# Performance work log

Measured on AMD Instinct MI355X. Metric: run time of the kernel, lower is better.

The kernel has to match this reference:

```python
import jax, jax.numpy as jnp
import numpy as np

K = 4096
CIN = 256


def _kaiming_uniform(key, shape):
    # torch kaiming_uniform_ default: gain=sqrt(2), bound = gain*sqrt(3/fan_in)
    fan_in = shape[1]
    bound = np.sqrt(6.0 / fan_in)
    return jax.random.uniform(key, shape, jnp.float32, -bound, bound)


def _linear_weight(key, shape):
    # torch nn.Linear default init: U(-1/sqrt(fan_in), 1/sqrt(fan_in))
    bound = 1.0 / np.sqrt(shape[1])
    return jax.random.uniform(key, shape, jnp.float32, -bound, bound)


def setup_inputs() -> dict:
    key = jax.random.key(0)
    k0, k1, k2, k3, k4 = jax.random.split(key, 5)
    latent = jax.random.normal(k0, (16, CIN, 32, 32), jnp.float32)
    temperature = jnp.float32(1.0)
    codebook = _kaiming_uniform(k1, (K, CIN))
    wq = _linear_weight(k2, (CIN, CIN))
    wk = _linear_weight(k3, (CIN, CIN))
    wv = _linear_weight(k4, (CIN, CIN))
    return {"latent": latent, "temperature": temperature, "codebook": codebook,
            "wq": wq, "wk": wk, "wv": wv}


def reference(latent, temperature, codebook, wq, wk, wv):
    # deterministic=True, additionWeight=True, dropout=None
    cin = latent.shape[1]
    scale = jnp.sqrt(jnp.asarray(cin, latent.dtype))
    q = jnp.einsum('nchw,dc->nhwd', latent, wq)      # [n,h,w,cin], Linear: x @ W^T
    kmat = codebook @ wk.T                           # [k,cin]
    v = codebook @ wv.T                              # [k,cin]
    logit = jnp.einsum('nhwc,kc->nhwk', q, kmat) / scale
    soft = jax.nn.softmax(logit, axis=-1)
    idx = jnp.argmax(logit, axis=-1)                 # [n,h,w]
    soft_v = jnp.einsum('nhwk,kc->nhwc', soft, v)
    hard_v = v[idx]                                  # one-hot @ v == gather
    result = jax.lax.stop_gradient(hard_v - soft_v) + soft_v
    quantized = jnp.transpose(result, (0, 3, 1, 2))  # [n,cin,h,w]
    return (quantized, idx.astype(jnp.uint8), logit, v)
```

## Files before the change

### kernel.cpp

```cpp
#include <hip/hip_runtime.h>
#include <math.h>
#include <float.h>

#define CIN 256
#define KCB 4096
#define NPOS 16384

#define OFF_QUANT 0
#define OFF_IDX   4194304
#define OFF_LOGIT 4210688
#define OFF_V     71319552

#define MARGIN 5e-4f

typedef short bf16x8 __attribute__((ext_vector_type(8)));
typedef float f32x4 __attribute__((ext_vector_type(4)));

__device__ __forceinline__ unsigned short rne_bf16(float x) {
  const unsigned u = __float_as_uint(x);
  return (unsigned short)((u + 0x7FFFu + ((u >> 16) & 1u)) >> 16);
}

__device__ __forceinline__ void gload_lds16(const void* g, void* l) {
  __builtin_amdgcn_global_load_lds(
      (const __attribute__((address_space(1))) unsigned int*)g,
      (__attribute__((address_space(3))) unsigned int*)l, 16, 0, 0);
}

__device__ __forceinline__ void top2_merge(float& m1, int& i1, float& m2,
                                           float om1, int oi1, float om2) {
  if (om1 > m1 || (om1 == m1 && oi1 < i1)) {
    m2 = fmaxf(m1, om2);
    m1 = om1;
    i1 = oi1;
  } else {
    m2 = fmaxf(m2, fmaxf(om1, om2));
  }
}

__global__ __launch_bounds__(256) void kvq_kernel(
    const float* __restrict__ cb, const float* __restrict__ wk,
    const float* __restrict__ wv, const float* __restrict__ latent,
    const float* __restrict__ wq, unsigned short* __restrict__ kb,
    float* __restrict__ kf, float* __restrict__ vout,
    unsigned short* __restrict__ qb, float* __restrict__ qf) {
  __shared__ float sh[16][CIN];
  const int t = threadIdx.x;
  if (blockIdx.x < 256) {
    const int k0 = blockIdx.x * 16;
#pragma unroll
    for (int i = 0; i < 16; ++i)
      sh[i][t] = cb[(size_t)(k0 + i) * CIN + t];
    __syncthreads();
    float acck[16], accv[16];
#pragma unroll
    for (int r = 0; r < 16; ++r) { acck[r] = 0.f; accv[r] = 0.f; }
    const float* wkr = wk + (size_t)t * CIN;
    const float* wvr = wv + (size_t)t * CIN;
    for (int j4 = 0; j4 < CIN; j4 += 4) {
      const float4 a4 = *(const float4*)&wkr[j4];
      const float4 b4 = *(const float4*)&wvr[j4];
      const float ae[4] = {a4.x, a4.y, a4.z, a4.w};
      const float be[4] = {b4.x, b4.y, b4.z, b4.w};
#pragma unroll
      for (int e = 0; e < 4; ++e) {
        const int j = j4 + e;
#pragma unroll
        for (int r = 0; r < 16; ++r) {
          const float c = sh[r][j];
          acck[r] = fmaf(c, ae[e], acck[r]);
          accv[r] = fmaf(c, be[e], accv[r]);
        }
      }
    }
#pragma unroll
    for (int r = 0; r < 16; ++r) {
      const float xk = acck[r];
      kb[(size_t)(k0 + r) * CIN + t] = rne_bf16(xk);
      kf[(size_t)(k0 + r) * CIN + t] = xk;
      vout[(size_t)(k0 + r) * CIN + t] = accv[r];
    }
  } else {
    const int p0 = (blockIdx.x - 256) * 16;
    const int n = p0 >> 10, hw0 = p0 & 1023;
    const float* lbase =
        latent + (size_t)n * (CIN * 1024) + (size_t)t * 1024 + hw0;
#pragma unroll
    for (int i4 = 0; i4 < 4; ++i4) {
      float4 v4 = *(const float4*)(lbase + i4 * 4);
      sh[i4 * 4 + 0][t] = v4.x;
      sh[i4 * 4 + 1][t] = v4.y;
      sh[i4 * 4 + 2][t] = v4.z;
      sh[i4 * 4 + 3][t] = v4.w;
    }
    __syncthreads();
    float acc[16];
#pragma unroll
    for (int r = 0; r < 16; ++r) acc[r] = 0.f;
    const float* wqr = wq + (size_t)t * CIN;
    for (int j4 = 0; j4 < CIN; j4 += 4) {
      const float4 w4 = *(const float4*)&wqr[j4];
      const float we[4] = {w4.x, w4.y, w4.z, w4.w};
#pragma unroll
      for (int e = 0; e < 4; ++e) {
        const int j = j4 + e;
#pragma unroll
        for (int r = 0; r < 16; ++r) acc[r] = fmaf(sh[r][j], we[e], acc[r]);
      }
    }
#pragma unroll
    for (int r = 0; r < 16; ++r) {
      qb[(size_t)(p0 + r) * CIN + t] = rne_bf16(acc[r]);
      qf[(size_t)(p0 + r) * CIN + t] = acc[r];
    }
  }
}

__global__ __launch_bounds__(256, 4) void logit_kernel(
    const unsigned short* __restrict__ qb, const unsigned short* __restrict__ kb,
    float* __restrict__ logit, float* __restrict__ pm1,
    int* __restrict__ pi1, float* __restrict__ pm2) {
  __shared__ __align__(16) unsigned short smem[2][2][128 * 32];

  const int t = threadIdx.x;
  const int b = blockIdx.x;
  const int x = (b & 7) * 512 + (b >> 3);
  const int bn = x & 31, bm = x >> 5;
  const int n0 = bn * 128, m0 = bm * 128;

  const int lane = t & 63, w = t >> 6;
  const int wr = w >> 1, wc = w & 1;
  const int fr = lane & 15, fq = lane >> 4;

  const int srow = t >> 2;
  const int spc = t & 3;
  const int slog = spc ^ ((srow >> 1) & 3);
  const int sldse = srow * 32 + spc * 8;

  int aoff[4], boff[4];
#pragma unroll
  for (int mi = 0; mi < 4; ++mi) {
    const int ar = wr * 64 + mi * 16 + fr;
    aoff[mi] = ar * 32 + (fq ^ ((ar >> 1) & 3)) * 8;
  }
#pragma unroll
  for (int ni = 0; ni < 4; ++ni) {
    const int br = wc * 64 + ni * 16 + fr;
    boff[ni] = br * 32 + (fq ^ ((br >> 1) & 3)) * 8;
  }

  f32x4 acc[4][4];
#pragma unroll
  for (int i = 0; i < 4; ++i)
#pragma unroll
    for (int j = 0; j < 4; ++j) acc[i][j] = (f32x4)(0.f);

#pragma unroll
  for (int h = 0; h < 2; ++h) {
    const int r = h * 64 + srow;
    gload_lds16(qb + (size_t)(m0 + r) * CIN + slog * 8,
                &smem[0][0][h * 2048 + sldse]);
    gload_lds16(kb + (size_t)(n0 + r) * CIN + slog * 8,
                &smem[0][1][h * 2048 + sldse]);
  }
  asm volatile("s_waitcnt vmcnt(0)" ::: "memory");
  __syncthreads();

  for (int s = 0; s < 8; ++s) {
    const int buf = s & 1;
    if (s < 7) {
      const int k0 = (s + 1) * 32;
      const int nb = buf ^ 1;
#pragma unroll
      for (int h = 0; h < 2; ++h) {
        const int r = h * 64 + srow;
        gload_lds16(qb + (size_t)(m0 + r) * CIN + k0 + slog * 8,
                    &smem[nb][0][h * 2048 + sldse]);
        gload_lds16(kb + (size_t)(n0 + r) * CIN + k0 + slog * 8,
                    &smem[nb][1][h * 2048 + sldse]);
      }
    }
    bf16x8 a[4], bfr[4];
#pragma unroll
    for (int mi = 0; mi < 4; ++mi) a[mi] = *(const bf16x8*)&smem[buf][0][aoff[mi]];
#pragma unroll
    for (int ni = 0; ni < 4; ++ni) bfr[ni] = *(const bf16x8*)&smem[buf][1][boff[ni]];
#pragma unroll
    for (int mi = 0; mi < 4; ++mi)
#pragma unroll
      for (int ni = 0; ni < 4; ++ni)
        acc[mi][ni] = __builtin_amdgcn_mfma_f32_16x16x32_bf16(
            a[mi], bfr[ni], acc[mi][ni], 0, 0, 0);
    asm volatile("s_waitcnt vmcnt(0)" ::: "memory");
    __syncthreads();
  }

  const float sc = 0.0625f;
  float* S1 = (float*)&smem[0][0][0];
  unsigned* S2 = (unsigned*)((char*)&smem[0][0][0] + 16384);
#pragma unroll
  for (int mi = 0; mi < 4; ++mi)
#pragma unroll
    for (int i = 0; i < 4; ++i) {
      const int rt = wr * 64 + mi * 16 + fq * 4 + i;
      const int row = m0 + rt;
      float vals[4];
#pragma unroll
      for (int ni = 0; ni < 4; ++ni) {
        vals[ni] = acc[mi][ni][i] * sc;
        __builtin_nontemporal_store(
            vals[ni], &logit[(size_t)row * KCB + n0 + wc * 64 + ni * 16 + fr]);
      }
      float m1 = vals[0], m2 = -FLT_MAX;
      int ni1 = 0;
#pragma unroll
      for (int ni = 1; ni < 4; ++ni) {
        if (vals[ni] > m1) { m2 = m1; m1 = vals[ni]; ni1 = ni; }
        else if (vals[ni] > m2) m2 = vals[ni];
      }
      const int sb = (wc * 128 + rt) * 16 + fr;
      S1[sb] = m1;
      S2[sb] = (__float_as_uint(m2) & ~3u) | (unsigned)ni1;
    }
  __syncthreads();
  if (t < 128) {
    float m1 = -FLT_MAX, m2 = -FLT_MAX;
    int i1 = 0;
#pragma unroll
    for (int wc2 = 0; wc2 < 2; ++wc2)
#pragma unroll
      for (int f4 = 0; f4 < 4; ++f4) {
        const int base = (wc2 * 128 + t) * 16 + f4 * 4;
        const float4 am1 = *(const float4*)&S1[base];
        const uint4 au2 = *(const uint4*)&S2[base];
        const unsigned ue[4] = {au2.x, au2.y, au2.z, au2.w};
        const float me[4] = {am1.x, am1.y, am1.z, am1.w};
#pragma unroll
        for (int e = 0; e < 4; ++e) {
          const int col = wc2 * 64 + (int)(ue[e] & 3u) * 16 + f4 * 4 + e;
          top2_merge(m1, i1, m2, me[e], col, __uint_as_float(ue[e] & ~3u));
        }
      }
    pm1[(size_t)(m0 + t) * 32 + bn] = m1;
    pi1[(size_t)(m0 + t) * 32 + bn] = n0 + i1;
    pm2[(size_t)(m0 + t) * 32 + bn] = m2;
  }
}

__global__ __launch_bounds__(256) void finish_kernel(
    const float* __restrict__ pm1, const int* __restrict__ pi1,
    const float* __restrict__ pm2, const float* __restrict__ logit,
    const float* __restrict__ qf, const float* __restrict__ kf,
    const float* __restrict__ vout, float* __restrict__ outq,
    float* __restrict__ outidx) {
  __shared__ float s_rowmax[16];
  __shared__ int s_rowidx[16];
  __shared__ int s_flag[16];
  __shared__ int s_nflag;
  __shared__ int s_cnt[4];
  __shared__ int s_list[4][64];

  const int t = threadIdx.x;
  const int p0 = blockIdx.x * 16;
  if (t == 0) s_nflag = 0;
  __syncthreads();

  {
    const int r = t >> 4, l16 = t & 15;
    const int p = p0 + r;
    const size_t base = (size_t)p * 32;
    float m1 = pm1[base + l16], m2 = pm2[base + l16];
    int i1 = pi1[base + l16];
    top2_merge(m1, i1, m2, pm1[base + 16 + l16], pi1[base + 16 + l16],
               pm2[base + 16 + l16]);
#pragma unroll
    for (int mask = 1; mask < 16; mask <<= 1) {
      const float om1 = __shfl_xor(m1, mask, 64);
      const int oi1 = __shfl_xor(i1, mask, 64);
      const float om2 = __shfl_xor(m2, mask, 64);
      top2_merge(m1, i1, m2, om1, oi1, om2);
    }
    if (l16 == 0) {
      s_rowidx[r] = i1;
      s_rowmax[r] = m1;
      if (m1 - m2 <= MARGIN) {
        const int pos = atomicAdd(&s_nflag, 1);
        s_flag[pos] = r;
      }
    }
  }
  __syncthreads();

  const int w = t >> 6, lane = t & 63;
  const int nf = s_nflag;
  for (int fi = w; fi < nf; fi += 4) {
    const int rloc = s_flag[fi];
    const int p = p0 + rloc;
    const float4 qv = *(const float4*)&qf[(size_t)p * CIN + lane * 4];
    if (lane == 0) s_cnt[w] = 0;
    const float thr = s_rowmax[rloc] - MARGIN;
    const float* lrow = logit + (size_t)p * KCB;
    for (int it = 0; it < 16; ++it) {
      const float4 xv = *(const float4*)&lrow[lane * 4 + it * 256];
      const float xe[4] = {xv.x, xv.y, xv.z, xv.w};
#pragma unroll
      for (int e = 0; e < 4; ++e) {
        if (xe[e] > thr) {
          const int pos = atomicAdd(&s_cnt[w], 1);
          if (pos < 64) s_list[w][pos] = lane * 4 + it * 256 + e;
        }
      }
    }
    const int nc = min(s_cnt[w], 64);
    float bestv = -FLT_MAX;
    int bestj = 0x7fffffff;
    for (int ci = 0; ci < nc; ++ci) {
      const int j = s_list[w][ci];
      const float4 kv4 = *(const float4*)&kf[(size_t)j * CIN + lane * 4];
      float d = qv.x * kv4.x + qv.y * kv4.y + qv.z * kv4.z + qv.w * kv4.w;
#pragma unroll
      for (int m = 1; m < 64; m <<= 1) d += __shfl_xor(d, m, 64);
      const float val = d * 0.0625f;
      if (val > bestv || (val == bestv && j < bestj)) { bestv = val; bestj = j; }
    }
    if (lane == 0) s_rowidx[rloc] = bestj;
  }
  __syncthreads();

  const int n = p0 >> 10, hw0 = p0 & 1023;
  float res[16];
#pragma unroll
  for (int r2 = 0; r2 < 16; ++r2)
    res[r2] = vout[(size_t)s_rowidx[r2] * CIN + t];
  float* ob = outq + (size_t)n * (CIN * 1024) + (size_t)t * 1024 + hw0;
#pragma unroll
  for (int i4 = 0; i4 < 4; ++i4)
    *(float4*)&ob[i4 * 4] = make_float4(res[i4 * 4 + 0], res[i4 * 4 + 1],
                                        res[i4 * 4 + 2], res[i4 * 4 + 3]);
  if (t < 16) outidx[p0 + t] = (float)(s_rowidx[t] & 255);
}

extern "C" void kernel_launch(void* const* d_in, const int* in_sizes, int n_in,
                              void* d_out, int out_size, void* d_ws,
                              size_t ws_size, hipStream_t stream) {
  const float* latent = (const float*)d_in[0];
  const float* codebook = (const float*)d_in[2];
  const float* wq = (const float*)d_in[3];
  const float* wk = (const float*)d_in[4];
  const float* wv = (const float*)d_in[5];

  float* out = (float*)d_out;
  float* outq = out + OFF_QUANT;
  float* outidx = out + OFF_IDX;
  float* outlogit = out + OFF_LOGIT;
  float* outv = out + OFF_V;

  char* ws = (char*)d_ws;
  unsigned short* qb = (unsigned short*)(ws + 0);
  unsigned short* kb = (unsigned short*)(ws + 8388608);
  float* kf = (float*)(ws + 10485760);
  float* pm1 = (float*)(ws + 14680064);
  int* pi1 = (int*)(ws + 16777216);
  float* pm2 = (float*)(ws + 18874368);
  float* qf = (float*)(ws + 20971520);

  kvq_kernel<<<256 + NPOS / 16, 256, 0, stream>>>(codebook, wk, wv, latent, wq,
                                                  kb, kf, outv, qb, qf);
  logit_kernel<<<4096, 256, 0, stream>>>(qb, kb, outlogit, pm1, pi1, pm2);
  finish_kernel<<<NPOS / 16, 256, 0, stream>>>(pm1, pi1, pm2, outlogit, qf, kf,
                                               outv, outq, outidx);
}
```

Before: 167.0 us.

## Fuse finish stage into logit kernel via last-block-per-panel atomic counter

Removes the separate finish kernel launch. Each logit block increments a per-row-panel counter after writing its partial top-2 results. The last of the 32 column blocks for a panel then does the argmax reduction, the near-tie rescoring and the quantized/index writes for those 128 rows. This saves a launch and lets the finish work overlap the tail of the logit GEMM. In exchange, the finish work per panel is serialized in a single block and extra threadfences are added. The counters are zeroed in the first kernel.

```diff
diff --git a/kernel.cpp b/kernel.cpp
--- a/kernel.cpp
+++ b/kernel.cpp
@@ -43,9 +43,11 @@
     const float* __restrict__ wv, const float* __restrict__ latent,
     const float* __restrict__ wq, unsigned short* __restrict__ kb,
     float* __restrict__ kf, float* __restrict__ vout,
-    unsigned short* __restrict__ qb, float* __restrict__ qf) {
+    unsigned short* __restrict__ qb, float* __restrict__ qf,
+    int* __restrict__ panel_cnt) {
   __shared__ float sh[16][CIN];
   const int t = threadIdx.x;
+  if (blockIdx.x == 0 && t < 128) panel_cnt[t] = 0;
   if (blockIdx.x < 256) {
     const int k0 = blockIdx.x * 16;
 #pragma unroll
@@ -119,7 +121,10 @@
 __global__ __launch_bounds__(256, 4) void logit_kernel(
     const unsigned short* __restrict__ qb, const unsigned short* __restrict__ kb,
     float* __restrict__ logit, float* __restrict__ pm1,
-    int* __restrict__ pi1, float* __restrict__ pm2) {
+    int* __restrict__ pi1, float* __restrict__ pm2,
+    const float* __restrict__ qf, const float* __restrict__ kf,
+    const float* __restrict__ vout, float* __restrict__ outq,
+    float* __restrict__ outidx, int* __restrict__ panel_cnt) {
   __shared__ __align__(16) unsigned short smem[2][2][128 * 32];
 
   const int t = threadIdx.x;
@@ -245,14 +250,17 @@
     pi1[(size_t)(m0 + t) * 32 + bn] = n0 + i1;
     pm2[(size_t)(m0 + t) * 32 + bn] = m2;
   }
-}
-
-__global__ __launch_bounds__(256) void finish_kernel(
-    const float* __restrict__ pm1, const int* __restrict__ pi1,
-    const float* __restrict__ pm2, const float* __restrict__ logit,
-    const float* __restrict__ qf, const float* __restrict__ kf,
-    const float* __restrict__ vout, float* __restrict__ outq,
-    float* __restrict__ outidx) {
+  __syncthreads();
+
+  __shared__ int s_last;
+  if (t == 0) {
+    __threadfence();
+    s_last = (atomicAdd(&panel_cnt[bm], 1) == 31) ? 1 : 0;
+  }
+  __syncthreads();
+  if (!s_last) return;
+  __threadfence();
+
   __shared__ float s_rowmax[16];
   __shared__ int s_rowidx[16];
   __shared__ int s_flag[16];
@@ -260,84 +268,92 @@
   __shared__ int s_cnt[4];
   __shared__ int s_list[4][64];
 
-  const int t = threadIdx.x;
-  const int p0 = blockIdx.x * 16;
-  if (t == 0) s_nflag = 0;
-  __syncthreads();
-
-  {
-    const int r = t >> 4, l16 = t & 15;
-    const int p = p0 + r;
-    const size_t base = (size_t)p * 32;
-    float m1 = pm1[base + l16], m2 = pm2[base + l16];
-    int i1 = pi1[base + l16];
-    top2_merge(m1, i1, m2, pm1[base + 16 + l16], pi1[base + 16 + l16],
-               pm2[base + 16 + l16]);
-#pragma unroll
-    for (int mask = 1; mask < 16; mask <<= 1) {
-      const float om1 = __shfl_xor(m1, mask, 64);
-      const int oi1 = __shfl_xor(i1, mask, 64);
-      const float om2 = __shfl_xor(m2, mask, 64);
-      top2_merge(m1, i1, m2, om1, oi1, om2);
-    }
-    if (l16 == 0) {
-      s_rowidx[r] = i1;
-      s_rowmax[r] = m1;
-      if (m1 - m2 <= MARGIN) {
-        const int pos = atomicAdd(&s_nflag, 1);
-        s_flag[pos] = r;
-      }
-    }
-  }
-  __syncthreads();
-
-  const int w = t >> 6, lane = t & 63;
-  const int nf = s_nflag;
-  for (int fi = w; fi < nf; fi += 4) {
-    const int rloc = s_flag[fi];
-    const int p = p0 + rloc;
-    const float4 qv = *(const float4*)&qf[(size_t)p * CIN + lane * 4];
-    if (lane == 0) s_cnt[w] = 0;
-    const float thr = s_rowmax[rloc] - MARGIN;
-    const float* lrow = logit + (size_t)p * KCB;
-    for (int it = 0; it < 16; ++it) {
-      const float4 xv = *(const float4*)&lrow[lane * 4 + it * 256];
-      const float xe[4] = {xv.x, xv.y, xv.z, xv.w};
-#pragma unroll
-      for (int e = 0; e < 4; ++e) {
-        if (xe[e] > thr) {
-          const int pos = atomicAdd(&s_cnt[w], 1);
-          if (pos < 64) s_list[w][pos] = lane * 4 + it * 256 + e;
-        }
-      }
-    }
-    const int nc = min(s_cnt[w], 64);
-    float bestv = -FLT_MAX;
-    int bestj = 0x7fffffff;
-    for (int ci = 0; ci < nc; ++ci) {
-      const int j = s_list[w][ci];
-      const float4 kv4 = *(const float4*)&kf[(size_t)j * CIN + lane * 4];
-      float d = qv.x * kv4.x + qv.y * kv4.y + qv.z * kv4.z + qv.w * kv4.w;
-#pragma unroll
-      for (int m = 1; m < 64; m <<= 1) d += __shfl_xor(d, m, 64);
-      const float val = d * 0.0625f;
-      if (val > bestv || (val == bestv && j < bestj)) { bestv = val; bestj = j; }
-    }
-    if (lane == 0) s_rowidx[rloc] = bestj;
-  }
-  __syncthreads();
-
-  const int n = p0 >> 10, hw0 = p0 & 1023;
-  float res[16];
-#pragma unroll
-  for (int r2 = 0; r2 < 16; ++r2)
-    res[r2] = vout[(size_t)s_rowidx[r2] * CIN + t];
-  float* ob = outq + (size_t)n * (CIN * 1024) + (size_t)t * 1024 + hw0;
-#pragma unroll
-  for (int i4 = 0; i4 < 4; ++i4)
-    *(float4*)&ob[i4 * 4] = make_float4(res[i4 * 4 + 0], res[i4 * 4 + 1],
-                                        res[i4 * 4 + 2], res[i4 * 4 + 3]);
-  if (t < 16) outidx[p0 + t] = (float)(s_rowidx[t] & 255);
+  for (int g = 0; g < 8; ++g) {
+    const int p0 = bm * 128 + g * 16;
+    if (t == 0) s_nflag = 0;
+    __syncthreads();
+
+    {
+      const int r = t >> 4, l16 = t & 15;
+      const int p = p0 + r;
+      const size_t base2 = (size_t)p * 32;
+      float m1 = pm1[base2 + l16], m2 = pm2[base2 + l16];
+      int i1 = pi1[base2 + l16];
+      top2_merge(m1, i1, m2, pm1[base2 + 16 + l16], pi1[base2 + 16 + l16],
+                 pm2[base2 + 16 + l16]);
+#pragma unroll
+      for (int mask = 1; mask < 16; mask <<= 1) {
+        const float om1 = __shfl_xor(m1, mask, 64);
+        const int oi1 = __shfl_xor(i1, mask, 64);
+        const float om2 = __shfl_xor(m2, mask, 64);
+        top2_merge(m1, i1, m2, om1, oi1, om2);
+      }
+      if (l16 == 0) {
+        s_rowidx[r] = i1;
+        s_rowmax[r] = m1;
+        if (m1 - m2 <= MARGIN) {
+          const int pos = atomicAdd(&s_nflag, 1);
+          s_flag[pos] = r;
+        }
+      }
+    }
+    __syncthreads();
+
+    {
+      const int nf = s_nflag;
+      for (int fi = w; fi < nf; fi += 4) {
+        const int rloc = s_flag[fi];
+        const int p = p0 + rloc;
+        const float4 qv = *(const float4*)&qf[(size_t)p * CIN + lane * 4];
+        if (lane == 0) s_cnt[w] = 0;
+        const float thr = s_rowmax[rloc] - MARGIN;
+        const float* lrow = logit + (size_t)p * KCB;
+        for (int it = 0; it < 16; ++it) {
+          const float4 xv = *(const float4*)&lrow[lane * 4 + it * 256];
+          const float xe[4] = {xv.x, xv.y, xv.z, xv.w};
+#pragma unroll
+          for (int e = 0; e < 4; ++e) {
+            if (xe[e] > thr) {
+              const int pos = atomicAdd(&s_cnt[w], 1);
+              if (pos < 64) s_list[w][pos] = lane * 4 + it * 256 + e;
+            }
+          }
+        }
+        const int nc = min(s_cnt[w], 64);
+        float bestv = -FLT_MAX;
+        int bestj = 0x7fffffff;
+        for (int ci = 0; ci < nc; ++ci) {
+          const int j = s_list[w][ci];
+          const float4 kv4 = *(const float4*)&kf[(size_t)j * CIN + lane * 4];
+          float d = qv.x * kv4.x + qv.y * kv4.y + qv.z * kv4.z + qv.w * kv4.w;
+#pragma unroll
+          for (int m = 1; m < 64; m <<= 1) d += __shfl_xor(d, m, 64);
+          const float val = d * 0.0625f;
+          if (val > bestv || (val == bestv && j < bestj)) {
+            bestv = val;
+            bestj = j;
+          }
+        }
+        if (lane == 0) s_rowidx[rloc] = bestj;
+      }
+    }
+    __syncthreads();
+
+    {
+      const int n = p0 >> 10, hw0 = p0 & 1023;
+      float res[16];
+#pragma unroll
+      for (int r2 = 0; r2 < 16; ++r2)
+        res[r2] = vout[(size_t)s_rowidx[r2] * CIN + t];
+      float* ob = outq + (size_t)n * (CIN * 1024) + (size_t)t * 1024 + hw0;
+#pragma unroll
+      for (int i4 = 0; i4 < 4; ++i4)
+        *(float4*)&ob[i4 * 4] = make_float4(res[i4 * 4 + 0], res[i4 * 4 + 1],
+                                            res[i4 * 4 + 2], res[i4 * 4 + 3]);
+      if (t < 16) outidx[p0 + t] = (float)(s_rowidx[t] & 255);
+    }
+    __syncthreads();
+  }
 }
 
 extern "C" void kernel_launch(void* const* d_in, const int* in_sizes, int n_in,
@@ -363,10 +379,11 @@
   int* pi1 = (int*)(ws + 16777216);
   float* pm2 = (float*)(ws + 18874368);
   float* qf = (float*)(ws + 20971520);
+  int* panel_cnt = (int*)(ws + 37748736);
 
   kvq_kernel<<<256 + NPOS / 16, 256, 0, stream>>>(codebook, wk, wv, latent, wq,
-                                                  kb, kf, outv, qb, qf);
-  logit_kernel<<<4096, 256, 0, stream>>>(qb, kb, outlogit, pm1, pi1, pm2);
-  finish_kernel<<<NPOS / 16, 256, 0, stream>>>(pm1, pi1, pm2, outlogit, qf, kf,
-                                               outv, outq, outidx);
-}
+                                                  kb, kf, outv, qb, qf,
+                                                  panel_cnt);
+  logit_kernel<<<4096, 256, 0, stream>>>(qb, kb, outlogit, pm1, pi1, pm2, qf,
+                                         kf, outv, outq, outidx, panel_cnt);
+}
```

Result: slower. 484.0 us (+189.8%).
